# Performance work log

Measured on AMD Instinct MI355X. Metric: run time of the kernel, lower is better.

## Reference

```python
import jax, jax.numpy as jnp
import numpy as np

B, H, G = 65536, 256, 7  # batch, hidden_dim, number of gates


def setup_inputs() -> dict:
    key = jax.random.key(0)
    k0, k1, k2, k3, k4, k5 = jax.random.split(key, 6)
    inter_times = jax.random.uniform(k0, (B,), dtype=jnp.float32)
    h_ti = jax.random.uniform(k1, (B, H), dtype=jnp.float32)
    c_ti = jax.random.uniform(k2, (B, H), dtype=jnp.float32)
    cbar = jax.random.uniform(k3, (B, H), dtype=jnp.float32)
    # 7 gate Linear layers stacked: order = input, forget, output, ibar, fbar, z, decay
    W = jax.random.normal(k4, (G, H, H), dtype=jnp.float32) * (1.0 / np.sqrt(H))
    b = jax.random.normal(k5, (G, H), dtype=jnp.float32) * 0.02
    return {"inter_times": inter_times, "h_ti": h_ti, "c_ti": c_ti, "cbar": cbar, "W": W, "b": b}


def reference(inter_times, h_ti, c_ti, cbar, W, b):
    # Batched GEMM for all 7 gates at once: torch Linear computes x @ W.T + b
    gates = jnp.einsum('bh,goh->gbo', h_ti, W) + b[:, None, :]  # [7,B,H]
    i_g = jax.nn.sigmoid(gates[0])
    f_g = jax.nn.sigmoid(gates[1])
    o_g = jax.nn.sigmoid(gates[2])
    ibar_g = jax.nn.sigmoid(gates[3])
    fbar_g = jax.nn.sigmoid(gates[4])
    z = jnp.tanh(gates[5])
    decay_t = jax.nn.softplus(gates[6])
    # decayed cell memory c(t) = cbar + (c - cbar) * exp(-decay * dt)
    dt = inter_times[:, None]  # [B,1]
    c_t_after = cbar + (c_ti - cbar) * jnp.exp(-decay_t * dt)
    c_new = f_g * c_t_after + i_g * z
    cbar_new = fbar_g * cbar + ibar_g * z
    h_new = o_g * jnp.tanh(c_t_after)
    return (o_g, h_new, c_new, cbar_new, decay_t)
```

## Files before the change

kernel.cpp:

```cpp
#include <hip/hip_runtime.h>
#include <hip/hip_bf16.h>
#include <cstddef>

#define BATCH 65536
#define HDIM  256
#define NGATE 7
#define BH    ((size_t)BATCH * HDIM)

typedef __bf16 bf16x8 __attribute__((ext_vector_type(8)));
typedef __bf16 bf16x4 __attribute__((ext_vector_type(4)));
typedef float  f32x4  __attribute__((ext_vector_type(4)));

__global__ void __launch_bounds__(256) cvt_w_kernel(const float* __restrict__ W,
                                                    __bf16* __restrict__ Wb) {
    int i = (blockIdx.x * 256 + threadIdx.x) * 4;
    float4 v = *(const float4*)(W + i);
    bf16x4 r;
    r[0] = (__bf16)v.x; r[1] = (__bf16)v.y; r[2] = (__bf16)v.z; r[3] = (__bf16)v.w;
    *(bf16x4*)(Wb + i) = r;
}

__device__ __forceinline__ float sigmoidf_(float x) {
    return __builtin_amdgcn_rcpf(1.0f + __expf(-x));
}
__device__ __forceinline__ float tanhf_(float x) {
    return 1.0f - 2.0f * __builtin_amdgcn_rcpf(1.0f + __expf(2.0f * x));
}
__device__ __forceinline__ float softplusf_(float x) {
    return fmaxf(x, 0.0f) + __logf(1.0f + __expf(-fabsf(x)));
}

__global__ void __launch_bounds__(256, 4)
fused_ctlstm(const float* __restrict__ inter_times,
             const float* __restrict__ h_ti,
             const float* __restrict__ c_ti,
             const float* __restrict__ cbar,
             const __bf16* __restrict__ Wb,
             const float* __restrict__ bias,
             float* __restrict__ out) {
    const int tid  = threadIdx.x;
    const int lane = tid & 63;
    const int wave = tid >> 6;
    const int col  = lane & 15;
    const int quad = lane >> 4;

    const int b = blockIdx.x * 64 + wave * 16 + col;
    const float dt = inter_times[b];

    bf16x8 bfrag[8];
    {
        const float* hp = h_ti + (size_t)b * HDIM + quad * 8;
#pragma unroll
        for (int ks = 0; ks < 8; ++ks) {
            float4 lo = *(const float4*)(hp + ks * 32);
            float4 hi = *(const float4*)(hp + ks * 32 + 4);
            bf16x8 v;
            v[0] = (__bf16)lo.x; v[1] = (__bf16)lo.y;
            v[2] = (__bf16)lo.z; v[3] = (__bf16)lo.w;
            v[4] = (__bf16)hi.x; v[5] = (__bf16)hi.y;
            v[6] = (__bf16)hi.z; v[7] = (__bf16)hi.w;
            bfrag[ks] = v;
        }
    }

#pragma unroll 1
    for (int ot = 0; ot < 16; ++ot) {
        const int o0   = ot * 16;
        const int orow = o0 + quad * 4;
        const size_t idx = (size_t)b * HDIM + orow;

        const f32x4 ct4 = *(const f32x4*)(c_ti + idx);
        const f32x4 cb4 = *(const f32x4*)(cbar + idx);

        f32x4 acc[NGATE];
#pragma unroll
        for (int g = 0; g < NGATE; ++g) acc[g] = (f32x4){0.f, 0.f, 0.f, 0.f};

#pragma unroll
        for (int ks = 0; ks < 8; ++ks) {
            const __bf16* wp = Wb + (size_t)(o0 + col) * HDIM + ks * 32 + quad * 8;
#pragma unroll
            for (int g = 0; g < NGATE; ++g) {
                bf16x8 afrag = *(const bf16x8*)(wp + (size_t)g * HDIM * HDIM);
                acc[g] = __builtin_amdgcn_mfma_f32_16x16x32_bf16(
                    afrag, bfrag[ks], acc[g], 0, 0, 0);
            }
        }

#pragma unroll
        for (int g = 0; g < NGATE; ++g)
            acc[g] += *(const f32x4*)(bias + g * HDIM + orow);

        f32x4 og4, hn4, cn4, cbn4, dec4;
#pragma unroll
        for (int r = 0; r < 4; ++r) {
            const float i_g  = sigmoidf_(acc[0][r]);
            const float f_g  = sigmoidf_(acc[1][r]);
            const float o_g  = sigmoidf_(acc[2][r]);
            const float ib_g = sigmoidf_(acc[3][r]);
            const float fb_g = sigmoidf_(acc[4][r]);
            const float z    = tanhf_(acc[5][r]);
            const float dec  = softplusf_(acc[6][r]);

            const float ct = ct4[r];
            const float cb = cb4[r];

            const float c_after = cb + (ct - cb) * __expf(-dec * dt);
            og4[r]  = o_g;
            hn4[r]  = o_g * tanhf_(c_after);
            cn4[r]  = f_g * c_after + i_g * z;
            cbn4[r] = fb_g * cb + ib_g * z;
            dec4[r] = dec;
        }

        __builtin_nontemporal_store(og4,  (f32x4*)(out + idx));
        __builtin_nontemporal_store(hn4,  (f32x4*)(out + BH + idx));
        __builtin_nontemporal_store(cn4,  (f32x4*)(out + 2 * BH + idx));
        __builtin_nontemporal_store(cbn4, (f32x4*)(out + 3 * BH + idx));
        __builtin_nontemporal_store(dec4, (f32x4*)(out + 4 * BH + idx));
    }
}

extern "C" void kernel_launch(void* const* d_in, const int* in_sizes, int n_in,
                              void* d_out, int out_size, void* d_ws, size_t ws_size,
                              hipStream_t stream) {
    const float* inter_times = (const float*)d_in[0];
    const float* h_ti        = (const float*)d_in[1];
    const float* c_ti        = (const float*)d_in[2];
    const float* cbar        = (const float*)d_in[3];
    const float* W           = (const float*)d_in[4];
    const float* bias        = (const float*)d_in[5];
    float* out = (float*)d_out;

    __bf16* Wb = (__bf16*)d_ws;

    cvt_w_kernel<<<(NGATE * HDIM * HDIM) / (256 * 4), 256, 0, stream>>>(W, Wb);

    fused_ctlstm<<<BATCH / 64, 256, 0, stream>>>(inter_times, h_ti, c_ti, cbar,
                                                 Wb, bias, out);
}
```

Before: 823.3 us.

## Tile output columns per block with LDS-resident swizzled weights and batch loop

Each block now owns a 16-column output tile and stages that tile's weights for all 7 gates in LDS with an XOR swizzle. It then loops over 1024 batch rows, prefetching the next h rows into registers. This replaces per-MFMA global weight loads with LDS reads, and bias is now loaded into the accumulators at init. In exchange, each h row is reread by all 16 column-tile blocks, and register and LDS pressure rise, so occupancy drops to 2 blocks per CU.

```diff
diff --git a/kernel.cpp b/kernel.cpp
--- a/kernel.cpp
+++ b/kernel.cpp
@@ -6,6 +6,15 @@
 #define HDIM  256
 #define NGATE 7
 #define BH    ((size_t)BATCH * HDIM)
+
+#define OTILE 16
+#define WAVES 4
+#define BPW   16
+#define BITER (WAVES * BPW)
+#define NITER 16
+#define BGRP  (BITER * NITER)
+#define NOT   (HDIM / OTILE)
+#define NBG   (BATCH / BGRP)
 
 typedef __bf16 bf16x8 __attribute__((ext_vector_type(8)));
 typedef __bf16 bf16x4 __attribute__((ext_vector_type(4)));
@@ -30,7 +39,7 @@
     return fmaxf(x, 0.0f) + __logf(1.0f + __expf(-fabsf(x)));
 }
 
-__global__ void __launch_bounds__(256, 4)
+__global__ void __launch_bounds__(256, 2)
 fused_ctlstm(const float* __restrict__ inter_times,
              const float* __restrict__ h_ti,
              const float* __restrict__ c_ti,
@@ -38,22 +47,59 @@
              const __bf16* __restrict__ Wb,
              const float* __restrict__ bias,
              float* __restrict__ out) {
+    __shared__ __bf16 wlds[NGATE * OTILE * HDIM];
+
     const int tid  = threadIdx.x;
     const int lane = tid & 63;
     const int wave = tid >> 6;
     const int col  = lane & 15;
     const int quad = lane >> 4;
 
-    const int b = blockIdx.x * 64 + wave * 16 + col;
-    const float dt = inter_times[b];
+    const int ot = blockIdx.x & (NOT - 1);
+    const int bg = blockIdx.x / NOT;
+    const int o0 = ot * OTILE;
 
-    bf16x8 bfrag[8];
+#pragma unroll
+    for (int r = 0; r < 14; ++r) {
+        int idx = r * 256 + tid;
+        int g   = idx >> 9;
+        int rem = idx & 511;
+        int o   = rem >> 5;
+        int kv  = rem & 31;
+        bf16x8 v = *(const bf16x8*)(Wb + ((size_t)g * HDIM + o0 + o) * HDIM + kv * 8);
+        int byte = (g * OTILE + o) * (HDIM * 2) + ((kv * 16) ^ ((o & 7) << 4));
+        *(bf16x8*)((char*)wlds + byte) = v;
+    }
+
+    const int orow = o0 + quad * 4;
+    f32x4 bv4[NGATE];
+#pragma unroll
+    for (int g = 0; g < NGATE; ++g)
+        bv4[g] = *(const f32x4*)(bias + g * HDIM + orow);
+
+    __syncthreads();
+
+    const int   swz  = (col & 7) << 4;
+    const char* wrow = (const char*)wlds + col * (HDIM * 2);
+
+    int b = bg * BGRP + wave * BPW + col;
+
+    float4 hv[16];
     {
         const float* hp = h_ti + (size_t)b * HDIM + quad * 8;
 #pragma unroll
         for (int ks = 0; ks < 8; ++ks) {
-            float4 lo = *(const float4*)(hp + ks * 32);
-            float4 hi = *(const float4*)(hp + ks * 32 + 4);
+            hv[2 * ks]     = *(const float4*)(hp + ks * 32);
+            hv[2 * ks + 1] = *(const float4*)(hp + ks * 32 + 4);
+        }
+    }
+
+#pragma unroll 1
+    for (int it = 0; it < NITER; ++it) {
+        bf16x8 bfrag[8];
+#pragma unroll
+        for (int ks = 0; ks < 8; ++ks) {
+            float4 lo = hv[2 * ks], hi = hv[2 * ks + 1];
             bf16x8 v;
             v[0] = (__bf16)lo.x; v[1] = (__bf16)lo.y;
             v[2] = (__bf16)lo.z; v[3] = (__bf16)lo.w;
@@ -61,35 +107,35 @@
             v[6] = (__bf16)hi.z; v[7] = (__bf16)hi.w;
             bfrag[ks] = v;
         }
-    }
 
-#pragma unroll 1
-    for (int ot = 0; ot < 16; ++ot) {
-        const int o0   = ot * 16;
-        const int orow = o0 + quad * 4;
         const size_t idx = (size_t)b * HDIM + orow;
-
         const f32x4 ct4 = *(const f32x4*)(c_ti + idx);
         const f32x4 cb4 = *(const f32x4*)(cbar + idx);
+        const float dt  = inter_times[b];
+
+        if (it + 1 < NITER) {
+            const float* hp = h_ti + (size_t)(b + BITER) * HDIM + quad * 8;
+#pragma unroll
+            for (int ks = 0; ks < 8; ++ks) {
+                hv[2 * ks]     = *(const float4*)(hp + ks * 32);
+                hv[2 * ks + 1] = *(const float4*)(hp + ks * 32 + 4);
+            }
+        }
 
         f32x4 acc[NGATE];
 #pragma unroll
-        for (int g = 0; g < NGATE; ++g) acc[g] = (f32x4){0.f, 0.f, 0.f, 0.f};
+        for (int g = 0; g < NGATE; ++g) acc[g] = bv4[g];
 
 #pragma unroll
         for (int ks = 0; ks < 8; ++ks) {
-            const __bf16* wp = Wb + (size_t)(o0 + col) * HDIM + ks * 32 + quad * 8;
+            const int ko = (((ks * 4 + quad) * 16) ^ swz);
 #pragma unroll
             for (int g = 0; g < NGATE; ++g) {
-                bf16x8 afrag = *(const bf16x8*)(wp + (size_t)g * HDIM * HDIM);
+                bf16x8 afrag = *(const bf16x8*)(wrow + g * (OTILE * HDIM * 2) + ko);
                 acc[g] = __builtin_amdgcn_mfma_f32_16x16x32_bf16(
                     afrag, bfrag[ks], acc[g], 0, 0, 0);
             }
         }
-
-#pragma unroll
-        for (int g = 0; g < NGATE; ++g)
-            acc[g] += *(const f32x4*)(bias + g * HDIM + orow);
 
         f32x4 og4, hn4, cn4, cbn4, dec4;
 #pragma unroll
@@ -118,6 +164,8 @@
         __builtin_nontemporal_store(cn4,  (f32x4*)(out + 2 * BH + idx));
         __builtin_nontemporal_store(cbn4, (f32x4*)(out + 3 * BH + idx));
         __builtin_nontemporal_store(dec4, (f32x4*)(out + 4 * BH + idx));
+
+        b += BITER;
     }
 }
 
@@ -136,6 +184,6 @@
 
     cvt_w_kernel<<<(NGATE * HDIM * HDIM) / (256 * 4), 256, 0, stream>>>(W, Wb);
 
-    fused_ctlstm<<<BATCH / 64, 256, 0, stream>>>(inter_times, h_ti, c_ti, cbar,
-                                                 Wb, bias, out);
+    fused_ctlstm<<<NOT * NBG, 256, 0, stream>>>(inter_times, h_ti, c_ti, cbar,
+                                                Wb, bias, out);
 }
```

New measurement: 971.1 us. +17.9%, slower.
